# Performance work log

Hardware: AMD Instinct MI355X
Metric: run time of the kernel (lower is better)

## Reference

```python
import jax, jax.numpy as jnp
import numpy as np

H = 8
D = 64  # head_dim = node_dim // num_heads = 512 // 8
NODE = 512
EPS = 1e-5


def setup_inputs() -> dict:
    key = jax.random.key(0)
    ks = jax.random.split(key, 8)
    S, IN = 4096, 1024
    return {
        "protT5_emb": jax.random.normal(ks[0], (S, IN), jnp.float32),
        "contact_matrix": jax.random.uniform(ks[1], (S, S), jnp.float32),
        "Wq": jax.random.normal(ks[2], (NODE, IN), jnp.float32) * 0.02,
        "bq": jnp.zeros((NODE,), jnp.float32),
        "Wk": jax.random.normal(ks[3], (NODE, IN), jnp.float32) * 0.02,
        "bk": jnp.zeros((NODE,), jnp.float32),
        "Wv": jax.random.normal(ks[4], (NODE, IN), jnp.float32) * 0.02,
        "bv": jnp.zeros((NODE,), jnp.float32),
        "Wc": jnp.ones((1, H, 1, 1), jnp.float32),
        "Wo": jax.random.normal(ks[5], (NODE, NODE), jnp.float32) * 0.02,
        "bo": jnp.zeros((NODE,), jnp.float32),
        "gamma": jnp.ones((NODE,), jnp.float32),
        "beta": jnp.zeros((NODE,), jnp.float32),
    }


def reference(protT5_emb, contact_matrix, Wq, bq, Wk, bk, Wv, bv, Wc, Wo, bo, gamma, beta):
    S = protT5_emb.shape[0]
    # QKV projections -> [H, S, D]
    Q = (protT5_emb @ Wq.T + bq).reshape(S, H, D).transpose(1, 0, 2)
    K = (protT5_emb @ Wk.T + bk).reshape(S, H, D).transpose(1, 0, 2)
    V = (protT5_emb @ Wv.T + bv).reshape(S, H, D).transpose(1, 0, 2)
    # raw scores [H, S, S]
    attn_raw = jnp.einsum('hsd,htd->hst', Q, K) / jnp.sqrt(jnp.float32(D))
    # multiplicative contact mask, per-head learnable scale
    contact_mask = contact_matrix[None, :, :] * Wc.reshape(H, 1, 1)
    attn_weight = jax.nn.softmax(attn_raw * contact_mask, axis=-1)
    attn_output = jnp.einsum('hst,htd->hsd', attn_weight, V)  # [H, S, D]
    # FAITHFUL to torch: transpose(0,1).view(S,-1) on [1,H,S,D] flattens in
    # (head, seq, dim) order -> scrambled [S, H*D] reshape, not head concat.
    attn_output = attn_output.reshape(S, H * D)
    aug = attn_output @ Wo.T + bo
    x = aug + protT5_emb[:, :NODE]
    mu = jnp.mean(x, axis=-1, keepdims=True)
    var = jnp.mean((x - mu) ** 2, axis=-1, keepdims=True)
    return (x - mu) * jax.lax.rsqrt(var + EPS) * gamma + beta
```

## Files before the change

kernel.cpp:

```cpp
#include <hip/hip_runtime.h>
#include <stdint.h>

#define SEQ 4096
#define INDIM 1024
#define NODEDIM 512
#define NH 8
#define HD 64
#define LSTR 72

typedef __bf16 bf16x8 __attribute__((ext_vector_type(8)));
typedef float f32x4 __attribute__((ext_vector_type(4)));

#define GLOAD_LDS(gp, lp) \
    __builtin_amdgcn_global_load_lds( \
        (const __attribute__((address_space(1))) void*)(gp), \
        (__attribute__((address_space(3))) void*)(lp), 16, 0, 0)

__device__ __forceinline__ unsigned short f2bf(float f) {
    union { float f; uint32_t u; } v; v.f = f;
    uint32_t u = v.u;
    uint32_t r = (u + 0x7fffu + ((u >> 16) & 1u)) >> 16;
    return (unsigned short)r;
}

__device__ __forceinline__ float fast_exp2(float x) {
    float r;
    asm volatile("v_exp_f32 %0, %1" : "=v"(r) : "v"(x));
    return r;
}

__global__ __launch_bounds__(256) void cvt_all(const float* __restrict__ emb,
                                               const float* __restrict__ Wq,
                                               const float* __restrict__ Wk,
                                               const float* __restrict__ Wv,
                                               const float* __restrict__ Wo,
                                               unsigned short* __restrict__ demb,
                                               unsigned short* __restrict__ dwqkv,
                                               unsigned short* __restrict__ dwo) {
    int b = blockIdx.x;
    const float* src;
    unsigned short* dst;
    int off;
    if (b < 4096)      { src = emb; dst = demb;            off = b; }
    else if (b < 4608) { src = Wq;  dst = dwqkv;           off = b - 4096; }
    else if (b < 5120) { src = Wk;  dst = dwqkv + 524288;  off = b - 4608; }
    else if (b < 5632) { src = Wv;  dst = dwqkv + 1048576; off = b - 5120; }
    else               { src = Wo;  dst = dwo;             off = b - 5632; }
    int i = (off * 256 + threadIdx.x) * 4;
    float4 v = *(const float4*)(src + i);
    ushort4 o;
    o.x = f2bf(v.x); o.y = f2bf(v.y); o.z = f2bf(v.z); o.w = f2bf(v.w);
    *(ushort4*)(dst + i) = o;
}

__global__ __launch_bounds__(256) void qkv_gemm(const unsigned short* __restrict__ A,
                                                const unsigned short* __restrict__ B,
                                                const float* __restrict__ bq,
                                                const float* __restrict__ bk,
                                                const float* __restrict__ bv,
                                                unsigned short* __restrict__ Qo,
                                                unsigned short* __restrict__ Ko,
                                                unsigned short* __restrict__ VTo) {
    __shared__ unsigned short As[128 * 32];
    __shared__ unsigned short Bs[128 * 32];
    __shared__ unsigned short Ts[128 * 40];
    const int tid = threadIdx.x;
    const int lane = tid & 63, wave = tid >> 6;
    const int wm = wave >> 1, wn = wave & 1;
    const int quad = lane >> 4, l16 = lane & 15;
    const int m0 = blockIdx.x * 128;
    const int n0 = blockIdx.y * 128;

    const int srow = tid >> 2, sqq = tid & 3;

    f32x4 acc[4][4] = {};

    for (int k0 = 0; k0 < INDIM; k0 += 32) {
        __syncthreads();
        for (int i = 0; i < 2; ++i) {
            int row = srow + 64 * i;
            GLOAD_LDS(A + (size_t)(m0 + row) * INDIM + k0 + sqq * 8, &As[row * 32 + sqq * 8]);
            GLOAD_LDS(B + (size_t)(n0 + row) * INDIM + k0 + sqq * 8, &Bs[row * 32 + sqq * 8]);
        }
        __syncthreads();
        bf16x8 af[4], bf[4];
        for (int mi = 0; mi < 4; ++mi)
            af[mi] = *(const bf16x8*)&As[(wm * 64 + mi * 16 + l16) * 32 + quad * 8];
        for (int ni = 0; ni < 4; ++ni)
            bf[ni] = *(const bf16x8*)&Bs[(wn * 64 + ni * 16 + l16) * 32 + quad * 8];
        for (int mi = 0; mi < 4; ++mi)
            for (int ni = 0; ni < 4; ++ni)
                acc[mi][ni] = __builtin_amdgcn_mfma_f32_16x16x32_bf16(af[mi], bf[ni], acc[mi][ni], 0, 0, 0);
    }

    if (blockIdx.y < 8) {
        unsigned short* outp = (blockIdx.y < 4) ? Qo : Ko;
        const float* biasp = (blockIdx.y < 4) ? bq : bk;
        for (int mi = 0; mi < 4; ++mi)
            for (int ni = 0; ni < 4; ++ni)
                for (int r = 0; r < 4; ++r) {
                    int s = m0 + wm * 64 + mi * 16 + quad * 4 + r;
                    int n = n0 + wn * 64 + ni * 16 + l16;
                    int h = (n >> 6) & 7;
                    int dd = n & 63;
                    float v = acc[mi][ni][r] + biasp[n & 511];
                    outp[((size_t)h * SEQ + s) * HD + dd] = f2bf(v);
                }
    } else {
        for (int chunk = 0; chunk < 4; ++chunk) {
            const int cwm = chunk >> 1;
            const int milo = (chunk & 1) * 2;
            __syncthreads();
            if (wm == cwm) {
                for (int mi2 = 0; mi2 < 2; ++mi2) {
                    int mi = milo + mi2;
                    for (int ni = 0; ni < 4; ++ni) {
                        int ddf = wn * 64 + ni * 16 + l16;
                        float bias = bv[(n0 + ddf) & 511];
                        for (int r = 0; r < 4; ++r) {
                            int sl = mi2 * 16 + quad * 4 + r;
                            Ts[ddf * 40 + sl] = f2bf(acc[mi][ni][r] + bias);
                        }
                    }
                }
            }
            __syncthreads();
            for (int pass = 0; pass < 2; ++pass) {
                int c = pass * 256 + tid;
                int row = c >> 2, part = c & 3;
                int nfull = n0 + row;
                int h = (nfull >> 6) & 7, dd = nfull & 63;
                *(bf16x8*)(VTo + ((size_t)h * HD + dd) * SEQ + m0 + chunk * 32 + part * 8) =
                    *(const bf16x8*)&Ts[row * 40 + part * 8];
            }
        }
    }
}

__global__ __launch_bounds__(256, 2) void attn_kernel(const unsigned short* __restrict__ Q,
                                                      const unsigned short* __restrict__ K,
                                                      const unsigned short* __restrict__ VT,
                                                      const float* __restrict__ CM,
                                                      const float* __restrict__ Wc,
                                                      float* __restrict__ O0,
                                                      float* __restrict__ O1,
                                                      float* __restrict__ O2,
                                                      float* __restrict__ O3,
                                                      float* __restrict__ l0,
                                                      float* __restrict__ l1,
                                                      float* __restrict__ l2,
                                                      float* __restrict__ l3,
                                                      int nsplit) {
    __shared__ unsigned short QPs[128 * LSTR];
    __shared__ unsigned short Ks[2][64 * LSTR];
    __shared__ unsigned short Vs[2][64 * LSTR];
    const int tid = threadIdx.x;
    const int lane = tid & 63, wave = tid >> 6;
    const int quad = lane >> 4, l16 = lane & 15;
    const int h0 = blockIdx.y * 2, h1 = h0 + 1;
    const int q0 = blockIdx.x * 128;
    const int split = blockIdx.z;
    float* __restrict__ Op = (split == 0) ? O0 : (split == 1) ? O1 : (split == 2) ? O2 : O3;
    float* __restrict__ lp = (split == 0) ? l0 : (split == 1) ? l1 : (split == 2) ? l2 : l3;
    const float wch0 = Wc[h0] * 0.125f * 1.44269504f;
    const float wch1 = Wc[h1] * 0.125f * 1.44269504f;

    const int tcount = SEQ / nsplit;
    const int tbeg = split * tcount;
    const int tend = tbeg + tcount;

    bf16x8 a0[2][2], a1[2][2];
    for (int i = 0; i < 4; ++i) {
        int c = tid + 256 * i;
        int row = c >> 3, part = c & 7;
        bf16x8 v = *(const bf16x8*)(Q + ((size_t)h0 * SEQ + q0 + row) * HD + part * 8);
        for (int j = 0; j < 8; ++j) v[j] = (__bf16)((float)v[j] * wch0);
        *(bf16x8*)&QPs[row * LSTR + part * 8] = v;
    }
    __syncthreads();
    for (int mi = 0; mi < 2; ++mi) {
        a0[mi][0] = *(const bf16x8*)&QPs[(wave * 32 + mi * 16 + l16) * LSTR + quad * 8];
        a0[mi][1] = *(const bf16x8*)&QPs[(wave * 32 + mi * 16 + l16) * LSTR + 32 + quad * 8];
    }
    __syncthreads();
    for (int i = 0; i < 4; ++i) {
        int c = tid + 256 * i;
        int row = c >> 3, part = c & 7;
        bf16x8 v = *(const bf16x8*)(Q + ((size_t)h1 * SEQ + q0 + row) * HD + part * 8);
        for (int j = 0; j < 8; ++j) v[j] = (__bf16)((float)v[j] * wch1);
        *(bf16x8*)&QPs[row * LSTR + part * 8] = v;
    }
    __syncthreads();
    for (int mi = 0; mi < 2; ++mi) {
        a1[mi][0] = *(const bf16x8*)&QPs[(wave * 32 + mi * 16 + l16) * LSTR + quad * 8];
        a1[mi][1] = *(const bf16x8*)&QPs[(wave * 32 + mi * 16 + l16) * LSTR + 32 + quad * 8];
    }

    const int srow0 = tid >> 3, spart = tid & 7;
    const int srow1 = (tid + 256) >> 3;
    const size_t hoff = (size_t)SEQ * HD;
    const unsigned short* kp0 = K + ((size_t)h0 * SEQ + tbeg + srow0) * HD + spart * 8;
    const unsigned short* kp1 = K + ((size_t)h0 * SEQ + tbeg + srow1) * HD + spart * 8;
    const unsigned short* vp0 = VT + ((size_t)h0 * HD + srow0) * SEQ + tbeg + spart * 8;
    const unsigned short* vp1 = VT + ((size_t)h0 * HD + srow1) * SEQ + tbeg + spart * 8;
    bf16x8 kr0a = *(const bf16x8*)kp0;
    bf16x8 kr1a = *(const bf16x8*)kp1;
    bf16x8 vr0a = *(const bf16x8*)vp0;
    bf16x8 vr1a = *(const bf16x8*)vp1;
    bf16x8 kr0b = *(const bf16x8*)(kp0 + hoff);
    bf16x8 kr1b = *(const bf16x8*)(kp1 + hoff);
    bf16x8 vr0b = *(const bf16x8*)(vp0 + hoff);
    bf16x8 vr1b = *(const bf16x8*)(vp1 + hoff);

    f32x4 Oa[2][4] = {}, Ob[2][4] = {};
    float l_pa[2][4] = {}, l_pb[2][4] = {};
    const float* cmbase0 = CM + (size_t)(q0 + wave * 32 + quad * 4) * SEQ + l16;
    const float* cmbase1 = cmbase0 + (size_t)16 * SEQ;
    const int sw = (l16 >> 2) & 3;

    for (int t0 = tbeg; t0 < tend; t0 += 64) {
        float cmv[2][4][4];
        for (int r = 0; r < 4; ++r)
            for (int nt = 0; nt < 4; ++nt) {
                cmv[0][r][nt] = cmbase0[(size_t)r * SEQ + t0 + nt * 16];
                cmv[1][r][nt] = cmbase1[(size_t)r * SEQ + t0 + nt * 16];
            }

        __syncthreads();
        *(bf16x8*)&Ks[0][srow0 * LSTR + spart * 8] = kr0a;
        *(bf16x8*)&Ks[0][srow1 * LSTR + spart * 8] = kr1a;
        *(bf16x8*)&Vs[0][srow0 * LSTR + spart * 8] = vr0a;
        *(bf16x8*)&Vs[0][srow1 * LSTR + spart * 8] = vr1a;
        *(bf16x8*)&Ks[1][srow0 * LSTR + spart * 8] = kr0b;
        *(bf16x8*)&Ks[1][srow1 * LSTR + spart * 8] = kr1b;
        *(bf16x8*)&Vs[1][srow0 * LSTR + spart * 8] = vr0b;
        *(bf16x8*)&Vs[1][srow1 * LSTR + spart * 8] = vr1b;
        __syncthreads();

        if (t0 + 64 < tend) {
            int d = t0 + 64 - tbeg;
            kr0a = *(const bf16x8*)(kp0 + (size_t)d * HD);
            kr1a = *(const bf16x8*)(kp1 + (size_t)d * HD);
            vr0a = *(const bf16x8*)(vp0 + d);
            vr1a = *(const bf16x8*)(vp1 + d);
            kr0b = *(const bf16x8*)(kp0 + (size_t)d * HD + hoff);
            kr1b = *(const bf16x8*)(kp1 + (size_t)d * HD + hoff);
            vr0b = *(const bf16x8*)(vp0 + d + hoff);
            vr1b = *(const bf16x8*)(vp1 + d + hoff);
        }

        {
            f32x4 sc[2][4];
            for (int nt = 0; nt < 4; ++nt) {
                bf16x8 b0 = *(const bf16x8*)&Ks[0][(nt * 16 + l16) * LSTR + quad * 8];
                bf16x8 b1 = *(const bf16x8*)&Ks[0][(nt * 16 + l16) * LSTR + 32 + quad * 8];
                for (int mi = 0; mi < 2; ++mi) {
                    f32x4 z = {0.f, 0.f, 0.f, 0.f};
                    z = __builtin_amdgcn_mfma_f32_16x16x32_bf16(a0[mi][0], b0, z, 0, 0, 0);
                    z = __builtin_amdgcn_mfma_f32_16x16x32_bf16(a0[mi][1], b1, z, 0, 0, 0);
                    sc[mi][nt] = z;
                }
            }
            for (int mi = 0; mi < 2; ++mi)
                for (int r = 0; r < 4; ++r)
                    for (int nt = 0; nt < 4; ++nt) {
                        float pv = fast_exp2(sc[mi][nt][r] * cmv[mi][r][nt]);
                        l_pa[mi][r] += pv;
                        union { float f; uint32_t u; } pu; pu.f = pv;
                        QPs[(wave * 32 + mi * 16 + quad * 4 + r) * LSTR
                            + (((nt * 2 + (l16 >> 3)) ^ quad) << 3) + (l16 & 7)] =
                            (unsigned short)(pu.u >> 16);
                    }
            asm volatile("s_waitcnt lgkmcnt(0)" ::: "memory");
            bf16x8 pa[2][2];
            for (int mi = 0; mi < 2; ++mi) {
                pa[mi][0] = *(const bf16x8*)&QPs[(wave * 32 + mi * 16 + l16) * LSTR + ((quad ^ sw) << 3)];
                pa[mi][1] = *(const bf16x8*)&QPs[(wave * 32 + mi * 16 + l16) * LSTR + 32 + ((quad ^ sw) << 3)];
            }
            for (int nt = 0; nt < 4; ++nt) {
                bf16x8 vb0 = *(const bf16x8*)&Vs[0][(nt * 16 + l16) * LSTR + quad * 8];
                bf16x8 vb1 = *(const bf16x8*)&Vs[0][(nt * 16 + l16) * LSTR + 32 + quad * 8];
                for (int mi = 0; mi < 2; ++mi) {
                    f32x4 o = Oa[mi][nt];
                    o = __builtin_amdgcn_mfma_f32_16x16x32_bf16(pa[mi][0], vb0, o, 0, 0, 0);
                    o = __builtin_amdgcn_mfma_f32_16x16x32_bf16(pa[mi][1], vb1, o, 0, 0, 0);
                    Oa[mi][nt] = o;
                }
            }
        }
        {
            f32x4 sc[2][4];
            for (int nt = 0; nt < 4; ++nt) {
                bf16x8 b0 = *(const bf16x8*)&Ks[1][(nt * 16 + l16) * LSTR + quad * 8];
                bf16x8 b1 = *(const bf16x8*)&Ks[1][(nt * 16 + l16) * LSTR + 32 + quad * 8];
                for (int mi = 0; mi < 2; ++mi) {
                    f32x4 z = {0.f, 0.f, 0.f, 0.f};
                    z = __builtin_amdgcn_mfma_f32_16x16x32_bf16(a1[mi][0], b0, z, 0, 0, 0);
                    z = __builtin_amdgcn_mfma_f32_16x16x32_bf16(a1[mi][1], b1, z, 0, 0, 0);
                    sc[mi][nt] = z;
                }
            }
            for (int mi = 0; mi < 2; ++mi)
                for (int r = 0; r < 4; ++r)
                    for (int nt = 0; nt < 4; ++nt) {
                        float pv = fast_exp2(sc[mi][nt][r] * cmv[mi][r][nt]);
                        l_pb[mi][r] += pv;
                        union { float f; uint32_t u; } pu; pu.f = pv;
                        QPs[(wave * 32 + mi * 16 + quad * 4 + r) * LSTR
                            + (((nt * 2 + (l16 >> 3)) ^ quad) << 3) + (l16 & 7)] =
                            (unsigned short)(pu.u >> 16);
                    }
            asm volatile("s_waitcnt lgkmcnt(0)" ::: "memory");
            bf16x8 pa[2][2];
            for (int mi = 0; mi < 2; ++mi) {
                pa[mi][0] = *(const bf16x8*)&QPs[(wave * 32 + mi * 16 + l16) * LSTR + ((quad ^ sw) << 3)];
                pa[mi][1] = *(const bf16x8*)&QPs[(wave * 32 + mi * 16 + l16) * LSTR + 32 + ((quad ^ sw) << 3)];
            }
            for (int nt = 0; nt < 4; ++nt) {
                bf16x8 vb0 = *(const bf16x8*)&Vs[1][(nt * 16 + l16) * LSTR + quad * 8];
                bf16x8 vb1 = *(const bf16x8*)&Vs[1][(nt * 16 + l16) * LSTR + 32 + quad * 8];
                for (int mi = 0; mi < 2; ++mi) {
                    f32x4 o = Ob[mi][nt];
                    o = __builtin_amdgcn_mfma_f32_16x16x32_bf16(pa[mi][0], vb0, o, 0, 0, 0);
                    o = __builtin_amdgcn_mfma_f32_16x16x32_bf16(pa[mi][1], vb1, o, 0, 0, 0);
                    Ob[mi][nt] = o;
                }
            }
        }
    }

    for (int mi = 0; mi < 2; ++mi)
        for (int r = 0; r < 4; ++r) {
            float s = l_pa[mi][r];
            for (int off = 1; off < 16; off <<= 1) s += __shfl_xor(s, off);
            l_pa[mi][r] = s;
            float s2 = l_pb[mi][r];
            for (int off = 1; off < 16; off <<= 1) s2 += __shfl_xor(s2, off);
            l_pb[mi][r] = s2;
        }
    if (l16 == 0)
        for (int mi = 0; mi < 2; ++mi)
            for (int r = 0; r < 4; ++r) {
                int sg = q0 + wave * 32 + mi * 16 + quad * 4 + r;
                lp[(size_t)h0 * SEQ + sg] = l_pa[mi][r];
                lp[(size_t)h1 * SEQ + sg] = l_pb[mi][r];
            }
    for (int mi = 0; mi < 2; ++mi)
        for (int nt = 0; nt < 4; ++nt)
            for (int r = 0; r < 4; ++r) {
                int sg = q0 + wave * 32 + mi * 16 + quad * 4 + r;
                Op[((size_t)h0 * SEQ + sg) * HD + nt * 16 + l16] = Oa[mi][nt][r];
                Op[((size_t)h1 * SEQ + sg) * HD + nt * 16 + l16] = Ob[mi][nt][r];
            }
}

__global__ __launch_bounds__(256) void combine_kernel(const float* __restrict__ O0,
                                                      const float* __restrict__ O1,
                                                      const float* __restrict__ O2,
                                                      const float* __restrict__ O3,
                                                      const float* __restrict__ l0,
                                                      const float* __restrict__ l1,
                                                      const float* __restrict__ l2,
                                                      const float* __restrict__ l3,
                                                      int nsplit,
                                                      unsigned short* __restrict__ AO) {
    int idx = blockIdx.x * 256 + threadIdx.x;
    int e = idx * 4;
    int row = e >> 6;
    float4 a = *(const float4*)(O0 + e);
    float4 b = *(const float4*)(O1 + e);
    float x = a.x + b.x, y = a.y + b.y, z = a.z + b.z, w = a.w + b.w;
    float ls = l0[row] + l1[row];
    if (nsplit >= 3) {
        float4 c = *(const float4*)(O2 + e);
        x += c.x; y += c.y; z += c.z; w += c.w;
        ls += l2[row];
    }
    if (nsplit >= 4) {
        float4 d = *(const float4*)(O3 + e);
        x += d.x; y += d.y; z += d.z; w += d.w;
        ls += l3[row];
    }
    float linv = 1.f / ls;
    ushort4 o;
    o.x = f2bf(x * linv);
    o.y = f2bf(y * linv);
    o.z = f2bf(z * linv);
    o.w = f2bf(w * linv);
    *(ushort4*)(AO + e) = o;
}

__global__ __launch_bounds__(256) void out_gemm(const unsigned short* __restrict__ A,
                                                const unsigned short* __restrict__ B,
                                                const float* __restrict__ bo,
                                                const float* __restrict__ emb,
                                                float* __restrict__ X) {
    __shared__ unsigned short As[64 * 32];
    __shared__ unsigned short Bs[128 * 32];
    const int tid = threadIdx.x;
    const int lane = tid & 63, wave = tid >> 6;
    const int quad = lane >> 4, l16 = lane & 15;
    const int m0 = blockIdx.x * 64;
    const int n0 = blockIdx.y * 128;

    const int srow = tid >> 2, sqq = tid & 3;

    f32x4 acc[8] = {};

    for (int k0 = 0; k0 < NODEDIM; k0 += 32) {
        __syncthreads();
        GLOAD_LDS(A + (size_t)(m0 + srow) * NODEDIM + k0 + sqq * 8, &As[srow * 32 + sqq * 8]);
        for (int i = 0; i < 2; ++i) {
            int row = srow + 64 * i;
            GLOAD_LDS(B + (size_t)(n0 + row) * NODEDIM + k0 + sqq * 8, &Bs[row * 32 + sqq * 8]);
        }
        __syncthreads();
        bf16x8 af = *(const bf16x8*)&As[(wave * 16 + l16) * 32 + quad * 8];
        for (int ni = 0; ni < 8; ++ni) {
            bf16x8 bf = *(const bf16x8*)&Bs[(ni * 16 + l16) * 32 + quad * 8];
            acc[ni] = __builtin_amdgcn_mfma_f32_16x16x32_bf16(af, bf, acc[ni], 0, 0, 0);
        }
    }

    for (int ni = 0; ni < 8; ++ni)
        for (int r = 0; r < 4; ++r) {
            int s = m0 + wave * 16 + quad * 4 + r;
            int n = n0 + ni * 16 + l16;
            float v = acc[ni][r] + bo[n] + emb[(size_t)s * INDIM + n];
            X[(size_t)s * NODEDIM + n] = v;
        }
}

__global__ __launch_bounds__(256) void ln_kernel(const float* __restrict__ X,
                                                 const float* __restrict__ gamma,
                                                 const float* __restrict__ beta,
                                                 float* __restrict__ out) {
    const int s = blockIdx.x;
    const int n = threadIdx.x * 2;
    float2 v = *(const float2*)&X[(size_t)s * NODEDIM + n];
    float sum = v.x + v.y;
    float sq = v.x * v.x + v.y * v.y;
    for (int off = 32; off > 0; off >>= 1) {
        sum += __shfl_down(sum, off);
        sq += __shfl_down(sq, off);
    }
    __shared__ float ssum[4], ssq[4];
    const int wave = threadIdx.x >> 6, lane = threadIdx.x & 63;
    if (lane == 0) { ssum[wave] = sum; ssq[wave] = sq; }
    __syncthreads();
    float tsum = ssum[0] + ssum[1] + ssum[2] + ssum[3];
    float tsq = ssq[0] + ssq[1] + ssq[2] + ssq[3];
    float mu = tsum * (1.f / 512.f);
    float var = tsq * (1.f / 512.f) - mu * mu;
    float rstd = rsqrtf(var + 1e-5f);
    float2 g = *(const float2*)&gamma[n];
    float2 b = *(const float2*)&beta[n];
    float2 o;
    o.x = (v.x - mu) * rstd * g.x + b.x;
    o.y = (v.y - mu) * rstd * g.y + b.y;
    *(float2*)&out[(size_t)s * NODEDIM + n] = o;
}

extern "C" void kernel_launch(void* const* d_in, const int* in_sizes, int n_in,
                              void* d_out, int out_size, void* d_ws, size_t ws_size,
                              hipStream_t stream) {
    const float* emb = (const float*)d_in[0];
    const float* cm  = (const float*)d_in[1];
    const float* Wq  = (const float*)d_in[2];
    const float* bq  = (const float*)d_in[3];
    const float* Wk  = (const float*)d_in[4];
    const float* bk  = (const float*)d_in[5];
    const float* Wv  = (const float*)d_in[6];
    const float* bv  = (const float*)d_in[7];
    const float* Wc  = (const float*)d_in[8];
    const float* Wo  = (const float*)d_in[9];
    const float* bo  = (const float*)d_in[10];
    const float* gamma = (const float*)d_in[11];
    const float* beta  = (const float*)d_in[12];
    float* out = (float*)d_out;

    unsigned short* ws = (unsigned short*)d_ws;
    unsigned short* emb_bf  = ws;
    unsigned short* wqkv_bf = emb_bf + 4194304;
    unsigned short* wo_bf   = wqkv_bf + 1572864;
    unsigned short* Qb  = wo_bf + 262144;
    unsigned short* Kb  = Qb + 2097152;
    unsigned short* VTb = Kb + 2097152;
    unsigned short* AOb = VTb + 2097152;
    float* X = (float*)(AOb + 2097152);
    float* O0 = (float*)emb_bf;
    float* O1 = X;
    float* O2 = X + 2097152;
    float* O3 = O2 + 2097152;
    float* l0 = (float*)wqkv_bf;
    float* l1 = l0 + NH * SEQ;
    float* l2 = l1 + NH * SEQ;
    float* l3 = l2 + NH * SEQ;

    const size_t NEED4 = 54001664ull;
    const int nz = (ws_size >= NEED4) ? 4 : 2;

    cvt_all<<<5888, 256, 0, stream>>>(emb, Wq, Wk, Wv, Wo, emb_bf, wqkv_bf, wo_bf);

    qkv_gemm<<<dim3(32, 12), 256, 0, stream>>>(emb_bf, wqkv_bf, bq, bk, bv, Qb, Kb, VTb);
    attn_kernel<<<dim3(32, 4, nz), 256, 0, stream>>>(Qb, Kb, VTb, cm, Wc,
                                                     O0, O1, O2, O3, l0, l1, l2, l3, nz);
    combine_kernel<<<2048, 256, 0, stream>>>(O0, O1, O2, O3, l0, l1, l2, l3, nz, AOb);
    out_gemm<<<dim3(64, 4), 256, 0, stream>>>(AOb, wo_bf, bo, emb, X);
    ln_kernel<<<4096, 256, 0, stream>>>(X, gamma, beta, out);
}
```

Before: 252.0 us.

## Prefetch contact-mask tile one iteration ahead and batch both heads' PV MFMAs

```diff
diff --git a/kernel.cpp b/kernel.cpp
--- a/kernel.cpp
+++ b/kernel.cpp
@@ -152,6 +152,7 @@
                                                       float* __restrict__ l3,
                                                       int nsplit) {
     __shared__ unsigned short QPs[128 * LSTR];
+    __shared__ unsigned short Ps1[128 * LSTR];
     __shared__ unsigned short Ks[2][64 * LSTR];
     __shared__ unsigned short Vs[2][64 * LSTR];
     const int tid = threadIdx.x;
@@ -218,14 +219,14 @@
     const float* cmbase1 = cmbase0 + (size_t)16 * SEQ;
     const int sw = (l16 >> 2) & 3;
 
+    float cmv[2][4][4];
+    for (int r = 0; r < 4; ++r)
+        for (int nt = 0; nt < 4; ++nt) {
+            cmv[0][r][nt] = cmbase0[(size_t)r * SEQ + tbeg + nt * 16];
+            cmv[1][r][nt] = cmbase1[(size_t)r * SEQ + tbeg + nt * 16];
+        }
+
     for (int t0 = tbeg; t0 < tend; t0 += 64) {
-        float cmv[2][4][4];
-        for (int r = 0; r < 4; ++r)
-            for (int nt = 0; nt < 4; ++nt) {
-                cmv[0][r][nt] = cmbase0[(size_t)r * SEQ + t0 + nt * 16];
-                cmv[1][r][nt] = cmbase1[(size_t)r * SEQ + t0 + nt * 16];
-            }
-
         __syncthreads();
         *(bf16x8*)&Ks[0][srow0 * LSTR + spart * 8] = kr0a;
         *(bf16x8*)&Ks[0][srow1 * LSTR + spart * 8] = kr1a;
@@ -237,6 +238,7 @@
         *(bf16x8*)&Vs[1][srow1 * LSTR + spart * 8] = vr1b;
         __syncthreads();
 
+        float cmn[2][4][4];
         if (t0 + 64 < tend) {
             int d = t0 + 64 - tbeg;
             kr0a = *(const bf16x8*)(kp0 + (size_t)d * HD);
@@ -247,6 +249,11 @@
             kr1b = *(const bf16x8*)(kp1 + (size_t)d * HD + hoff);
             vr0b = *(const bf16x8*)(vp0 + d + hoff);
             vr1b = *(const bf16x8*)(vp1 + d + hoff);
+            for (int r = 0; r < 4; ++r)
+                for (int nt = 0; nt < 4; ++nt) {
+                    cmn[0][r][nt] = cmbase0[(size_t)r * SEQ + t0 + 64 + nt * 16];
+                    cmn[1][r][nt] = cmbase1[(size_t)r * SEQ + t0 + 64 + nt * 16];
+                }
         }
 
         {
@@ -271,22 +278,6 @@
                             + (((nt * 2 + (l16 >> 3)) ^ quad) << 3) + (l16 & 7)] =
                             (unsigned short)(pu.u >> 16);
                     }
-            asm volatile("s_waitcnt lgkmcnt(0)" ::: "memory");
-            bf16x8 pa[2][2];
-            for (int mi = 0; mi < 2; ++mi) {
-                pa[mi][0] = *(const bf16x8*)&QPs[(wave * 32 + mi * 16 + l16) * LSTR + ((quad ^ sw) << 3)];
-                pa[mi][1] = *(const bf16x8*)&QPs[(wave * 32 + mi * 16 + l16) * LSTR + 32 + ((quad ^ sw) << 3)];
-            }
-            for (int nt = 0; nt < 4; ++nt) {
-                bf16x8 vb0 = *(const bf16x8*)&Vs[0][(nt * 16 + l16) * LSTR + quad * 8];
-                bf16x8 vb1 = *(const bf16x8*)&Vs[0][(nt * 16 + l16) * LSTR + 32 + quad * 8];
-                for (int mi = 0; mi < 2; ++mi) {
-                    f32x4 o = Oa[mi][nt];
-                    o = __builtin_amdgcn_mfma_f32_16x16x32_bf16(pa[mi][0], vb0, o, 0, 0, 0);
-                    o = __builtin_amdgcn_mfma_f32_16x16x32_bf16(pa[mi][1], vb1, o, 0, 0, 0);
-                    Oa[mi][nt] = o;
-                }
-            }
         }
         {
             f32x4 sc[2][4];
@@ -306,27 +297,46 @@
                         float pv = fast_exp2(sc[mi][nt][r] * cmv[mi][r][nt]);
                         l_pb[mi][r] += pv;
                         union { float f; uint32_t u; } pu; pu.f = pv;
-                        QPs[(wave * 32 + mi * 16 + quad * 4 + r) * LSTR
+                        Ps1[(wave * 32 + mi * 16 + quad * 4 + r) * LSTR
                             + (((nt * 2 + (l16 >> 3)) ^ quad) << 3) + (l16 & 7)] =
                             (unsigned short)(pu.u >> 16);
                     }
-            asm volatile("s_waitcnt lgkmcnt(0)" ::: "memory");
-            bf16x8 pa[2][2];
+        }
+
+        asm volatile("s_waitcnt lgkmcnt(0)" ::: "memory");
+
+        {
+            bf16x8 pa[2][2], pb[2][2];
             for (int mi = 0; mi < 2; ++mi) {
                 pa[mi][0] = *(const bf16x8*)&QPs[(wave * 32 + mi * 16 + l16) * LSTR + ((quad ^ sw) << 3)];
                 pa[mi][1] = *(const bf16x8*)&QPs[(wave * 32 + mi * 16 + l16) * LSTR + 32 + ((quad ^ sw) << 3)];
+                pb[mi][0] = *(const bf16x8*)&Ps1[(wave * 32 + mi * 16 + l16) * LSTR + ((quad ^ sw) << 3)];
+                pb[mi][1] = *(const bf16x8*)&Ps1[(wave * 32 + mi * 16 + l16) * LSTR + 32 + ((quad ^ sw) << 3)];
             }
             for (int nt = 0; nt < 4; ++nt) {
-                bf16x8 vb0 = *(const bf16x8*)&Vs[1][(nt * 16 + l16) * LSTR + quad * 8];
-                bf16x8 vb1 = *(const bf16x8*)&Vs[1][(nt * 16 + l16) * LSTR + 32 + quad * 8];
+                bf16x8 vb0 = *(const bf16x8*)&Vs[0][(nt * 16 + l16) * LSTR + quad * 8];
+                bf16x8 vb1 = *(const bf16x8*)&Vs[0][(nt * 16 + l16) * LSTR + 32 + quad * 8];
+                bf16x8 wb0 = *(const bf16x8*)&Vs[1][(nt * 16 + l16) * LSTR + quad * 8];
+                bf16x8 wb1 = *(const bf16x8*)&Vs[1][(nt * 16 + l16) * LSTR + 32 + quad * 8];
                 for (int mi = 0; mi < 2; ++mi) {
-                    f32x4 o = Ob[mi][nt];
+                    f32x4 o = Oa[mi][nt];
                     o = __builtin_amdgcn_mfma_f32_16x16x32_bf16(pa[mi][0], vb0, o, 0, 0, 0);
                     o = __builtin_amdgcn_mfma_f32_16x16x32_bf16(pa[mi][1], vb1, o, 0, 0, 0);
-                    Ob[mi][nt] = o;
-                }
-            }
-        }
+                    Oa[mi][nt] = o;
+                    f32x4 p = Ob[mi][nt];
+                    p = __builtin_amdgcn_mfma_f32_16x16x32_bf16(pb[mi][0], wb0, p, 0, 0, 0);
+                    p = __builtin_amdgcn_mfma_f32_16x16x32_bf16(pb[mi][1], wb1, p, 0, 0, 0);
+                    Ob[mi][nt] = p;
+                }
+            }
+        }
+
+        if (t0 + 64 < tend)
+            for (int r = 0; r < 4; ++r)
+                for (int nt = 0; nt < 4; ++nt) {
+                    cmv[0][r][nt] = cmn[0][r][nt];
+                    cmv[1][r][nt] = cmn[1][r][nt];
+                }
     }
 
     for (int mi = 0; mi < 2; ++mi)
```

Result: slower. 289.9 us (+15.0%).
